# Kernel tuning notes

Measured on AMD Instinct MI355X. Metric: run time of the kernel, lower is better.

The kernel has to match this reference:

```python
import jax, jax.numpy as jnp
import numpy as np

B, C, H, W = 4, 96, 48, 48
N_STATE = 16
EXPAND = 2
D_INNER = EXPAND * C          # 192
DT_RANK = -(-C // 16)         # ceil(96/16) = 6
K = 4                         # 4 scan directions (VMamba cross-scan)
CA_R = 16                     # channel-attention reduction


def _ln(x, g, b, eps=1e-5):
    m = jnp.mean(x, -1, keepdims=True)
    v = jnp.mean((x - m) ** 2, -1, keepdims=True)
    return (x - m) * jax.lax.rsqrt(v + eps) * g + b


def setup_inputs() -> dict:
    key = jax.random.key(0)
    ks = jax.random.split(key, 12)
    f = lambda k, s, scale=0.02: jax.random.normal(k, s, dtype=jnp.float32) * scale
    # dt bias init per SS2D.dt_init: inv_dt = dt + log(-expm1(-dt))
    dt0 = jnp.exp(jax.random.uniform(ks[7], (K, D_INNER)) * (np.log(0.1) - np.log(1e-3)) + np.log(1e-3))
    dt_b = dt0 + jnp.log(-jnp.expm1(-dt0))
    A_logs = jnp.log(jnp.tile(jnp.arange(1, N_STATE + 1, dtype=jnp.float32)[None, :], (K * D_INNER, 1)))
    return {
        "x": jax.random.normal(ks[0], (B, C, H, W), dtype=jnp.float32),
        "ca_w1": f(ks[1], (C // CA_R, C), 0.1),
        "ca_w2": f(ks[2], (C, C // CA_R), 0.1),
        "ln_g": jnp.ones((C,), jnp.float32),
        "ln_b": jnp.zeros((C,), jnp.float32),
        "in_proj_w": f(ks[3], (2 * D_INNER, C)),
        "conv_w": f(ks[4], (D_INNER, 1, 3, 3), 0.1),
        "conv_b": jnp.zeros((D_INNER,), jnp.float32),
        "x_proj_w": f(ks[5], (K, DT_RANK + 2 * N_STATE, D_INNER)),
        "dt_w": f(ks[6], (K, D_INNER, DT_RANK), DT_RANK ** -0.5),
        "dt_b": dt_b,
        "A_logs": A_logs,
        "Ds": jnp.ones((K * D_INNER,), jnp.float32),
        "onorm_g": jnp.ones((D_INNER,), jnp.float32),
        "onorm_b": jnp.zeros((D_INNER,), jnp.float32),
        "out_proj_w": f(ks[8], (C, D_INNER)),
    }


def reference(x, ca_w1, ca_w2, ln_g, ln_b, in_proj_w, conv_w, conv_b,
              x_proj_w, dt_w, dt_b, A_logs, Ds, onorm_g, onorm_b, out_proj_w):
    # --- channel attention (SE-style) gating the encoder features ---
    s = x.mean((2, 3))                                    # [B,C]
    a = jax.nn.sigmoid(jax.nn.relu(s @ ca_w1.T) @ ca_w2.T)
    x_ca = x * a[:, :, None, None]

    # --- VSSBlock: LN -> SS2D -> residual ---
    xi = jnp.transpose(x_ca, (0, 2, 3, 1))               # [B,H,W,C]
    xn = _ln(xi, ln_g, ln_b)

    # SS2D in_proj, split x/z
    xz = xn @ in_proj_w.T                                 # [B,H,W,2*D]
    xc, z = jnp.split(xz, 2, axis=-1)

    # depthwise conv + SiLU
    xc = jnp.transpose(xc, (0, 3, 1, 2))                  # [B,D,H,W]
    xc = jax.lax.conv_general_dilated(
        xc, conv_w, (1, 1), 'SAME', feature_group_count=D_INNER,
        dimension_numbers=('NCHW', 'OIHW', 'NCHW')) + conv_b[None, :, None, None]
    xc = jax.nn.silu(xc)

    Bb, D, Hh, Ww = xc.shape
    L = Hh * Ww
    # cross-scan: hw, wh, and their reverses -> [B,4,D,L]
    x_hw = xc.reshape(Bb, D, L)
    x_wh = jnp.transpose(xc, (0, 1, 3, 2)).reshape(Bb, D, L)
    xs = jnp.stack([x_hw, x_wh], axis=1)
    xs = jnp.concatenate([xs, jnp.flip(xs, axis=-1)], axis=1)

    x_dbl = jnp.einsum('bkdl,kcd->bkcl', xs, x_proj_w)    # [B,4,R+2N,L]
    dts, Bs, Cs = jnp.split(x_dbl, [DT_RANK, DT_RANK + N_STATE], axis=2)
    dt = jnp.einsum('bkrl,kdr->bkdl', dts, dt_w)
    dt = jax.nn.softplus(dt + dt_b[None, :, :, None])     # [B,4,D,L]
    A = -jnp.exp(A_logs).reshape(K, D, N_STATE)           # [4,D,N]

    # selective scan over L (sequential recurrence, vectorized over B,K,D,N)
    dt_t = jnp.moveaxis(dt, -1, 0)                        # [L,B,4,D]
    B_t = jnp.moveaxis(Bs, -1, 0)                         # [L,B,4,N]
    C_t = jnp.moveaxis(Cs, -1, 0)
    u_t = jnp.moveaxis(xs, -1, 0)                         # [L,B,4,D]
    h0 = jnp.zeros((Bb, K, D, N_STATE), xc.dtype)

    def step(h, inp):
        dti, Bi, Ci, ui = inp
        h = h * jnp.exp(dti[..., None] * A) + (dti * ui)[..., None] * Bi[:, :, None, :]
        return h, jnp.einsum('bkdn,bkn->bkd', h, Ci)

    _, ys = jax.lax.scan(step, h0, (dt_t, B_t, C_t, u_t))
    ys = jnp.moveaxis(ys, 0, -1) + Ds.reshape(K, D)[None, :, :, None] * xs  # [B,4,D,L]

    # merge 4 directions back to hw order
    y_fwd, y_inv = ys[:, :2], jnp.flip(ys[:, 2:], axis=-1)

    def wh_to_hw(t):
        return jnp.transpose(t.reshape(Bb, D, Ww, Hh), (0, 1, 3, 2)).reshape(Bb, D, L)

    y = y_fwd[:, 0] + y_inv[:, 0] + wh_to_hw(y_fwd[:, 1]) + wh_to_hw(y_inv[:, 1])
    y = jnp.transpose(y.reshape(Bb, D, Hh, Ww), (0, 2, 3, 1))  # [B,H,W,D]
    y = _ln(y, onorm_g, onorm_b)
    y = y * jax.nn.silu(z)
    out = y @ out_proj_w.T                                # [B,H,W,C]
    out = xi + out                                        # VSSBlock residual
    return jnp.transpose(out, (0, 3, 1, 2))               # [B,C,H,W]
```

## Files before the change

### kernel.cpp

```cpp
#include <hip/hip_runtime.h>
#include <math.h>

#define Bn 4
#define Cc 96
#define Hh 48
#define Ww 48
#define HW 2304
#define Dd 192
#define NS 16
#define Kk 4
#define RK 6
#define CD 38
#define Ll 2304
#define NCH 64
#define CL 36
#define SU2S 72

typedef _Float16 half2v __attribute__((ext_vector_type(2)));
typedef _Float16 half4 __attribute__((ext_vector_type(4)));
typedef _Float16 half8 __attribute__((ext_vector_type(8)));
typedef float f4v __attribute__((ext_vector_type(4)));
typedef float f4raw __attribute__((ext_vector_type(4)));

#define FMA4(A,W,U) { A.x=fmaf(W,U.x,A.x); A.y=fmaf(W,U.y,A.y); A.z=fmaf(W,U.z,A.z); A.w=fmaf(W,U.w,A.w); }

__device__ __forceinline__ float sigmoidf_(float x){ return 1.0f/(1.0f+__expf(-x)); }
__device__ __forceinline__ float siluf_(float x){ return x*sigmoidf_(x); }
__device__ __forceinline__ float softplus_fast(float x){ return (x>15.0f)? x : __logf(1.0f+__expf(x)); }

__device__ __forceinline__ float dot2f(half2v a, half2v b, float c){
#if __has_builtin(__builtin_amdgcn_fdot2)
  return __builtin_amdgcn_fdot2(a, b, c, false);
#else
  return fmaf((float)a[1],(float)b[1], fmaf((float)a[0],(float)b[0], c));
#endif
}

__global__ __launch_bounds__(256) void k_mean(const float* __restrict__ x, float* __restrict__ s){
  int bc = blockIdx.x;
  const float* p = x + (size_t)bc*HW;
  float acc = 0.f;
  for(int i=threadIdx.x;i<HW;i+=256) acc += p[i];
  __shared__ float red[256];
  red[threadIdx.x]=acc; __syncthreads();
  for(int o=128;o>0;o>>=1){ if(threadIdx.x<o) red[threadIdx.x]+=red[threadIdx.x+o]; __syncthreads(); }
  if(threadIdx.x==0) s[bc]=red[0]*(1.0f/HW);
}

__global__ __launch_bounds__(384) void k_ca(const float* __restrict__ s, const float* __restrict__ w1,
                     const float* __restrict__ w2, float* __restrict__ a){
  __shared__ float hid[Bn*RK];
  int tid=threadIdx.x;
  if(tid<Bn*RK){
    int b=tid/RK, r=tid%RK;
    float acc=0.f;
    for(int c=0;c<Cc;c++) acc += s[b*Cc+c]*w1[r*Cc+c];
    hid[tid]=fmaxf(acc,0.f);
  }
  __syncthreads();
  int b=tid/Cc, c=tid%Cc;
  float acc=0.f;
  for(int r=0;r<RK;r++) acc += hid[b*RK+r]*w2[c*RK+r];
  a[tid]=sigmoidf_(acc);
}

__global__ __launch_bounds__(256) void k_xca(const float* __restrict__ x, const float* __restrict__ a,
                      float* __restrict__ xi){
  __shared__ float tile[32][65];
  int p0 = blockIdx.x*64, c0 = blockIdx.y*32, b = blockIdx.z;
  int pj = threadIdx.x%64, ci = threadIdx.x/64;
  for(int i=0;i<8;i++){
    int c = c0+ci+i*4;
    tile[ci+i*4][pj] = x[((size_t)(b*Cc+c))*HW + p0+pj]*a[b*Cc+c];
  }
  __syncthreads();
  int cl = threadIdx.x%32, pl = threadIdx.x/32;
  for(int i=0;i<8;i++){
    int p = pl + i*8;
    xi[((size_t)(b*HW + p0+p))*Cc + c0+cl] = tile[cl][p];
  }
}

__global__ __launch_bounds__(256) void k_lnproj(const float* __restrict__ xi,
    const float* __restrict__ g, const float* __restrict__ bta,
    const float* __restrict__ w, float* __restrict__ xc, float* __restrict__ z){
  __shared__ float su[Cc*36];
  __shared__ _Float16 wl16[128*104];
  int tid = threadIdx.x;
  int pix0 = blockIdx.x*32;
  int p = blockIdx.y;
  #pragma unroll
  for(int i=0;i<3;i++){
    int f4 = tid + 256*i;
    int px = f4/24, c4 = f4%24;
    float4 v = *(const float4*)(xi + (size_t)(pix0+px)*Cc + 4*c4);
    int sw = 4*(c4&7);
    su[(4*c4+0)*36 + (px^sw)] = v.x;
    su[(4*c4+1)*36 + (px^sw)] = v.y;
    su[(4*c4+2)*36 + (px^sw)] = v.z;
    su[(4*c4+3)*36 + (px^sw)] = v.w;
  }
  __syncthreads();
  {
    int px = tid>>3, gg = tid&7;
    float sm=0.f, sq=0.f;
    float vals[12];
    #pragma unroll
    for(int i=0;i<12;i++){
      int d = gg + 8*i;
      float v = su[d*36 + (px ^ (4*((d>>2)&7)))];
      vals[i]=v; sm+=v; sq+=v*v;
    }
    sm += __shfl_xor(sm,1); sq += __shfl_xor(sq,1);
    sm += __shfl_xor(sm,2); sq += __shfl_xor(sq,2);
    sm += __shfl_xor(sm,4); sq += __shfl_xor(sq,4);
    float mean = sm*(1.0f/Cc);
    float var  = sq*(1.0f/Cc) - mean*mean;
    float rs = rsqrtf(var + 1e-5f);
    #pragma unroll
    for(int i=0;i<12;i++){
      int d = gg + 8*i;
      su[d*36 + (px ^ (4*((d>>2)&7)))] = (vals[i]-mean)*rs*g[d] + bta[d];
    }
  }
  #pragma unroll
  for(int i=0;i<12;i++){
    int f4 = tid + 256*i;
    int r = f4/24, c4 = f4%24;
    float4 v = *(const float4*)(w + (size_t)(128*p + r)*Cc + 4*c4);
    half4 hv; hv[0]=(_Float16)v.x; hv[1]=(_Float16)v.y; hv[2]=(_Float16)v.z; hv[3]=(_Float16)v.w;
    *(half4*)(wl16 + r*104 + 4*c4) = hv;
  }
  __syncthreads();
  int t4 = tid&7, cg = tid>>3;
  float4 a0={0,0,0,0},a1={0,0,0,0},a2={0,0,0,0},a3={0,0,0,0};
  for(int d0=0; d0<Cc; d0+=8){
    half8 w0v = *(const half8*)(wl16 + (cg+  0)*104 + d0);
    half8 w1v = *(const half8*)(wl16 + (cg+ 32)*104 + d0);
    half8 w2v = *(const half8*)(wl16 + (cg+ 64)*104 + d0);
    half8 w3v = *(const half8*)(wl16 + (cg+ 96)*104 + d0);
    #pragma unroll
    for(int j=0;j<8;j++){
      int d = d0+j;
      float4 u4 = *(const float4*)(su + d*36 + 4*(t4 ^ ((d>>2)&7)));
      FMA4(a0,(float)w0v[j],u4);
      FMA4(a1,(float)w1v[j],u4);
      FMA4(a2,(float)w2v[j],u4);
      FMA4(a3,(float)w3v[j],u4);
    }
  }
  #pragma unroll
  for(int j=0;j<4;j++){
    int c = 128*p + cg + 32*j;
    float4 a = (j==0)?a0:(j==1)?a1:(j==2)?a2:a3;
    #pragma unroll
    for(int q=0;q<4;q++){
      int px = pix0 + 4*t4 + q;
      float vv = (q==0)?a.x:(q==1)?a.y:(q==2)?a.z:a.w;
      if(c < Dd) xc[(size_t)px*Dd + c] = vv;
      else       z [(size_t)px*Dd + (c-Dd)] = vv;
    }
  }
}

__global__ __launch_bounds__(256) void k_conv(const float* __restrict__ xc, const float* __restrict__ cw,
                       const float* __restrict__ cb, float* __restrict__ xo){
  int idx = blockIdx.x*256 + threadIdx.x;
  if(idx >= Bn*HW*(Dd/4)) return;
  int d4 = idx % (Dd/4); int pos = (idx/(Dd/4))%HW; int b = idx/((Dd/4)*HW);
  int h = pos/Ww, w = pos%Ww;
  int d0 = d4*4;
  float4 acc = {cb[d0],cb[d0+1],cb[d0+2],cb[d0+3]};
  #pragma unroll
  for(int kh=0;kh<3;kh++){
    int hh=h+kh-1; if(hh<0||hh>=Hh) continue;
    #pragma unroll
    for(int kw=0;kw<3;kw++){
      int ww2=w+kw-1; if(ww2<0||ww2>=Ww) continue;
      float4 v = *(const float4*)(xc + ((size_t)(b*HW + hh*Ww+ww2))*Dd + d0);
      int wi = kh*3+kw;
      acc.x += v.x*cw[(d0+0)*9+wi];
      acc.y += v.y*cw[(d0+1)*9+wi];
      acc.z += v.z*cw[(d0+2)*9+wi];
      acc.w += v.w*cw[(d0+3)*9+wi];
    }
  }
  float4 o; o.x=siluf_(acc.x); o.y=siluf_(acc.y); o.z=siluf_(acc.z); o.w=siluf_(acc.w);
  *(float4*)(xo + ((size_t)(b*HW+pos))*Dd + d0) = o;
}

__global__ __launch_bounds__(256) void k_xdbl(const float* __restrict__ xconv,
   const float* __restrict__ xpw, const float* __restrict__ dtw,
   const float* __restrict__ dtb, _Float16* __restrict__ dtC,
   _Float16* __restrict__ uC, _Float16* __restrict__ BC){
  __shared__ _Float16 su2[96*SU2S];
  __shared__ _Float16 wl16[CD*200];
  __shared__ float dts[RK*36];
  int tid = threadIdx.x;
  int blk = blockIdx.x;
  int tile = blk % (Ll/32);
  int k    = (blk/(Ll/32))%Kk;
  int b    = blk/((Ll/32)*Kk);
  int ord  = k&1;
  bool rev = (k>=2);
  int t0 = tile*32;
  #pragma unroll
  for(int i=0;i<6;i++){
    int f4 = tid+256*i;
    int r = f4/48, c4 = f4%48;
    int t = t0+r;
    int pos = ord ? ((t%Ww)*Ww + t/Ww) : t;
    float4 v = *(const float4*)(xconv + (size_t)(b*HW+pos)*Dd + 4*c4);
    int dp0 = 2*c4;
    int off = ((r>>2) ^ (c4&7))*8 + (r&3)*2;
    half2v p0; p0[0]=(_Float16)v.x; p0[1]=(_Float16)v.y;
    half2v p1; p1[0]=(_Float16)v.z; p1[1]=(_Float16)v.w;
    *(half2v*)(su2 + dp0*SU2S + off) = p0;
    *(half2v*)(su2 + (dp0+1)*SU2S + off) = p1;
    if(k<2){
      half4 hv; hv[0]=(_Float16)v.x; hv[1]=(_Float16)v.y; hv[2]=(_Float16)v.z; hv[3]=(_Float16)v.w;
      *(half4*)(uC + ((size_t)(b*2+ord)*Ll + t)*Dd + 4*c4) = hv;
    }
  }
  for(int i=tid;i<CD*48;i+=256){
    int c = i/48, c4 = i%48;
    float4 v = *(const float4*)(xpw + ((size_t)(k*CD+c))*Dd + 4*c4);
    half4 hv; hv[0]=(_Float16)v.x; hv[1]=(_Float16)v.y; hv[2]=(_Float16)v.z; hv[3]=(_Float16)v.w;
    *(half4*)(wl16 + c*200 + 4*c4) = hv;
  }
  __syncthreads();
  int t4 = tid&7, cg = tid>>3;
  bool has1 = (cg < CD-32);
  f4v a0={0,0,0,0}, a1={0,0,0,0};
  #pragma unroll 1
  for(int dpc=0; dpc<24; dpc++){
    f4raw w0r = *(const f4raw*)(wl16 + cg*200 + 8*dpc);
    f4raw w1r = {0.f,0.f,0.f,0.f};
    if(has1) w1r = *(const f4raw*)(wl16 + (cg+32)*200 + 8*dpc);
    #pragma unroll
    for(int j=0;j<4;j++){
      int dp = 4*dpc+j;
      f4raw ur = *(const f4raw*)(su2 + dp*SU2S + (t4 ^ ((dp>>1)&7))*8);
      half2v w0p = __builtin_bit_cast(half2v, w0r[j]);
      half2v w1p = __builtin_bit_cast(half2v, w1r[j]);
      #pragma unroll
      for(int q=0;q<4;q++){
        half2v up = __builtin_bit_cast(half2v, ur[q]);
        a0[q] = dot2f(up, w0p, a0[q]);
        if(has1) a1[q] = dot2f(up, w1p, a1[q]);
      }
    }
  }
  #pragma unroll
  for(int j=0;j<2;j++){
    if(j==1 && !has1) break;
    int c = cg + 32*j;
    f4v a = j? a1 : a0;
    if(c < RK){
      dts[c*36 + 4*t4+0]=a[0]; dts[c*36+4*t4+1]=a[1]; dts[c*36+4*t4+2]=a[2]; dts[c*36+4*t4+3]=a[3];
    } else {
      int nn = c - RK;
      _Float16* dst = BC + ((size_t)(b*Kk+k)*Ll)*32 + nn;
      #pragma unroll
      for(int q=0;q<4;q++){
        int t = t0 + 4*t4 + q;
        int tq = rev ? (Ll-1-t) : t;
        dst[(size_t)tq*32] = (_Float16)a[q];
      }
    }
  }
  __syncthreads();
  {
    int tl = tid&31, ds8 = tid>>5;
    #pragma unroll 4
    for(int i=0;i<24;i++){
      int d = ds8 + 8*i;
      float acc = dtb[k*Dd + d];
      #pragma unroll
      for(int r=0;r<RK;r++) acc = fmaf(dtw[((size_t)(k*Dd+d))*RK + r], dts[r*36 + tl], acc);
      wl16[tl*200 + d] = (_Float16)softplus_fast(acc);
    }
  }
  __syncthreads();
  {
    _Float16* dbase = dtC + (size_t)(b*Kk+k)*Ll*Dd;
    #pragma unroll
    for(int i=0;i<3;i++){
      int f8 = tid + 256*i;
      int row = f8/24, c8 = f8%24;
      int t = t0+row;
      int tq = rev ? (Ll-1-t) : t;
      *(half8*)(dbase + (size_t)tq*Dd + 8*c8) = *(const half8*)(wl16 + row*200 + 8*c8);
    }
  }
}

__global__ __launch_bounds__(192) void k_scan1(const _Float16* __restrict__ dtC,
  const _Float16* __restrict__ uC, const _Float16* __restrict__ BC,
  const float* __restrict__ Alog, _Float16* __restrict__ hloc, _Float16* __restrict__ Pb){
  int blk=blockIdx.x;
  int ch  = blk%NCH;
  int k   = (blk/NCH)%Kk;
  int b   = blk/(NCH*Kk);
  int d = threadIdx.x;
  const float* ap = Alog + ((size_t)(k*Dd+d))*NS;
  float An[16];
  #pragma unroll
  for(int i=0;i<16;i++) An[i] = -__expf(ap[i]);
  const _Float16* dp = dtC + (size_t)(b*Kk+k)*Ll*Dd + d;
  const _Float16* up = uC  + (size_t)(b*2+(k&1))*Ll*Dd + d;
  const _Float16* bc = BC  + ((size_t)(b*Kk+k)*Ll + ch*CL)*32;
  bool rev = (k>=2);
  int s0 = ch*CL;
  float h[16];
  #pragma unroll
  for(int i=0;i<16;i++) h[i]=0.f;
  float sdt = 0.f;
  #pragma unroll 1
  for(int tl=0; tl<CL; tl+=4){
    float dtv4[4], uv[4];
    #pragma unroll
    for(int j=0;j<4;j++){
      dtv4[j] = (float)dp[(size_t)(s0+tl+j)*Dd];
      int ut = rev ? (Ll-1-s0-tl-j) : (s0+tl+j);
      uv[j]  = (float)up[(size_t)ut*Dd];
    }
    #pragma unroll
    for(int j=0;j<4;j++){
      half8 B0 = *(const half8*)(bc + (size_t)(tl+j)*32);
      half8 B1 = *(const half8*)(bc + (size_t)(tl+j)*32 + 8);
      float dtv = dtv4[j];
      sdt += dtv;
      float xB = dtv*uv[j];
      #pragma unroll
      for(int i=0;i<8;i++){
        float ae = __expf(dtv*An[i]);
        h[i] = fmaf(h[i], ae, xB*(float)B0[i]);
      }
      #pragma unroll
      for(int i=0;i<8;i++){
        float ae = __expf(dtv*An[8+i]);
        h[8+i] = fmaf(h[8+i], ae, xB*(float)B1[i]);
      }
    }
  }
  size_t o = (((size_t)(b*Kk+k)*NCH + ch)*Dd + d)*NS;
  half8 ho0, ho1;
  #pragma unroll
  for(int i=0;i<8;i++){ ho0[i]=(_Float16)h[i]; ho1[i]=(_Float16)h[8+i]; }
  *(half8*)(hloc+o) = ho0; *(half8*)(hloc+o+8) = ho1;
  half8 po0, po1;
  #pragma unroll
  for(int i=0;i<8;i++){ po0[i]=(_Float16)__expf(An[i]*sdt); po1[i]=(_Float16)__expf(An[8+i]*sdt); }
  *(half8*)(Pb+o) = po0; *(half8*)(Pb+o+8) = po1;
}

__global__ __launch_bounds__(256) void k_comb(_Float16* __restrict__ hloc,
  const _Float16* __restrict__ Pb){
  int idx = blockIdx.x*256 + threadIdx.x;
  int inner = idx % (Dd*NS);
  int bk = idx / (Dd*NS);
  size_t base = (size_t)bk*NCH*Dd*NS + inner;
  float H = 0.f;
  for(int ch=0; ch<NCH; ch++){
    size_t o = base + (size_t)ch*Dd*NS;
    float hl = (float)hloc[o];
    hloc[o] = (_Float16)H;
    H = (float)Pb[o]*H + hl;
  }
}

__global__ __launch_bounds__(192) void k_scan2(const _Float16* __restrict__ dtC,
  const _Float16* __restrict__ uC, const _Float16* __restrict__ BC,
  const float* __restrict__ Alog, const float* __restrict__ Ds,
  const _Float16* __restrict__ Hin, _Float16* __restrict__ yB){
  int blk=blockIdx.x;
  int ch  = blk%NCH;
  int k   = (blk/NCH)%Kk;
  int b   = blk/(NCH*Kk);
  int d = threadIdx.x;
  const float* ap = Alog + ((size_t)(k*Dd+d))*NS;
  float An[16];
  #pragma unroll
  for(int i=0;i<16;i++) An[i] = -__expf(ap[i]);
  float Dv = Ds[k*Dd+d];
  const _Float16* dp = dtC + (size_t)(b*Kk+k)*Ll*Dd + d;
  const _Float16* up = uC  + (size_t)(b*2+(k&1))*Ll*Dd + d;
  const _Float16* bc = BC  + ((size_t)(b*Kk+k)*Ll + ch*CL)*32;
  bool rev = (k>=2);
  int s0 = ch*CL;
  const _Float16* hp = Hin + (((size_t)(b*Kk+k)*NCH + ch)*Dd + d)*NS;
  float h[16];
  {
    half8 h0=*(const half8*)(hp), h1=*(const half8*)(hp+8);
    #pragma unroll
    for(int i=0;i<8;i++){ h[i]=(float)h0[i]; h[8+i]=(float)h1[i]; }
  }
  _Float16* yp = yB + ((size_t)(b*Kk+k)*Ll + s0)*Dd + d;
  #pragma unroll 1
  for(int tl=0; tl<CL; tl+=4){
    float dtv4[4], uv[4];
    #pragma unroll
    for(int j=0;j<4;j++){
      dtv4[j] = (float)dp[(size_t)(s0+tl+j)*Dd];
      int ut = rev ? (Ll-1-s0-tl-j) : (s0+tl+j);
      uv[j]  = (float)up[(size_t)ut*Dd];
    }
    #pragma unroll
    for(int j=0;j<4;j++){
      half8 B0 = *(const half8*)(bc + (size_t)(tl+j)*32);
      half8 B1 = *(const half8*)(bc + (size_t)(tl+j)*32 + 8);
      half8 C0 = *(const half8*)(bc + (size_t)(tl+j)*32 + 16);
      half8 C1 = *(const half8*)(bc + (size_t)(tl+j)*32 + 24);
      float dtv = dtv4[j];
      float xB = dtv*uv[j];
      float p = 0.f;
      #pragma unroll
      for(int i=0;i<8;i++){
        float ae = __expf(dtv*An[i]);
        h[i] = fmaf(h[i], ae, xB*(float)B0[i]);
        p = fmaf(h[i], (float)C0[i], p);
      }
      #pragma unroll
      for(int i=0;i<8;i++){
        float ae = __expf(dtv*An[8+i]);
        h[8+i] = fmaf(h[8+i], ae, xB*(float)B1[i]);
        p = fmaf(h[8+i], (float)C1[i], p);
      }
      yp[(size_t)(tl+j)*Dd] = (_Float16)(p + Dv*uv[j]);
    }
  }
}

__global__ __launch_bounds__(256) void k_merge(const _Float16* __restrict__ yB,
  const float* __restrict__ og, const float* __restrict__ ob,
  const float* __restrict__ zB, const float* __restrict__ opw,
  const float* __restrict__ xi, float* __restrict__ ot){
  __shared__ float yv[Dd*36];
  __shared__ _Float16 wl16[48*200];
  int tid = threadIdx.x;
  int pix0 = blockIdx.x*32;
  int p = blockIdx.y;
  int b = pix0/HW;
  int pos0 = pix0%HW;
  size_t ybase = (size_t)b*Kk*Ll*Dd;
  #pragma unroll
  for(int i=0;i<3;i++){
    int f8 = tid+256*i;
    int r = f8/24, c8 = f8%24;
    int pos = pos0+r;
    int lwh = (pos%Ww)*Ww + pos/Ww;
    half8 v0 = *(const half8*)(yB + ybase + ((size_t)(0*Ll) + pos)*Dd + 8*c8);
    half8 v2 = *(const half8*)(yB + ybase + ((size_t)(2*Ll) + (Ll-1-pos))*Dd + 8*c8);
    half8 v1 = *(const half8*)(yB + ybase + ((size_t)(1*Ll) + lwh)*Dd + 8*c8);
    half8 v3 = *(const half8*)(yB + ybase + ((size_t)(3*Ll) + (Ll-1-lwh))*Dd + 8*c8);
    #pragma unroll
    for(int j=0;j<8;j++){
      int d = 8*c8+j;
      float vs = (float)v0[j]+(float)v1[j]+(float)v2[j]+(float)v3[j];
      yv[d*36 + (r ^ (4*((d>>2)&7)))] = vs;
    }
  }
  for(int i=tid;i<48*48;i+=256){
    int c=i/48, c4=i%48;
    float4 v = *(const float4*)(opw + (size_t)(48*p+c)*Dd + 4*c4);
    half4 hv; hv[0]=(_Float16)v.x; hv[1]=(_Float16)v.y; hv[2]=(_Float16)v.z; hv[3]=(_Float16)v.w;
    *(half4*)(wl16 + c*200 + 4*c4) = hv;
  }
  __syncthreads();
  {
    int px = tid>>3, gg = tid&7;
    float sm=0.f, sq=0.f;
    float vals[24];
    #pragma unroll
    for(int i=0;i<24;i++){
      int d = gg + 8*i;
      float v = yv[d*36 + (px ^ (4*((d>>2)&7)))];
      vals[i]=v; sm+=v; sq+=v*v;
    }
    sm += __shfl_xor(sm,1); sq += __shfl_xor(sq,1);
    sm += __shfl_xor(sm,2); sq += __shfl_xor(sq,2);
    sm += __shfl_xor(sm,4); sq += __shfl_xor(sq,4);
    float mean = sm*(1.0f/Dd);
    float var  = sq*(1.0f/Dd) - mean*mean;
    float rs = rsqrtf(var + 1e-5f);
    #pragma unroll
    for(int i=0;i<24;i++){
      int d = gg + 8*i;
      float zv = zB[(size_t)(pix0+px)*Dd + d];
      yv[d*36 + (px ^ (4*((d>>2)&7)))] = ((vals[i]-mean)*rs*og[d] + ob[d]) * siluf_(zv);
    }
  }
  __syncthreads();
  int t4 = tid&7, cg = tid>>3;
  bool h1 = (cg < 16);
  float4 a0={0,0,0,0}, a1={0,0,0,0};
  for(int d0=0;d0<Dd;d0+=8){
    half8 w0v = *(const half8*)(wl16 + cg*200 + d0);
    half8 w1v;
    if(h1) w1v = *(const half8*)(wl16 + (cg+32)*200 + d0);
    #pragma unroll
    for(int j=0;j<8;j++){
      int d=d0+j;
      float4 u4 = *(const float4*)(yv + d*36 + 4*(t4 ^ ((d>>2)&7)));
      FMA4(a0,(float)w0v[j],u4);
      if(h1){ FMA4(a1,(float)w1v[j],u4); }
    }
  }
  #pragma unroll
  for(int j=0;j<2;j++){
    if(j==1 && !h1) break;
    int c = 48*p + cg + 32*j;
    float4 a = j?a1:a0;
    #pragma unroll
    for(int q=0;q<4;q++){
      int px = pix0 + 4*t4 + q;
      float vv = (q==0)?a.x:(q==1)?a.y:(q==2)?a.z:a.w;
      ot[(size_t)px*Cc + c] = vv + xi[(size_t)px*Cc + c];
    }
  }
}

__global__ __launch_bounds__(256) void k_outT(const float* __restrict__ ot, float* __restrict__ out){
  __shared__ float tile[64][33];
  int p0=blockIdx.x*64, c0=blockIdx.y*32, b=blockIdx.z;
  int cl=threadIdx.x%32, pl=threadIdx.x/32;
  for(int i=0;i<8;i++){
    int p = pl+i*8;
    tile[p][cl] = ot[((size_t)(b*HW+p0+p))*Cc + c0+cl];
  }
  __syncthreads();
  int pj=threadIdx.x%64, ci=threadIdx.x/64;
  for(int i=0;i<8;i++){
    int c=ci+i*4;
    out[((size_t)(b*Cc+c0+c))*HW + p0+pj] = tile[pj][c];
  }
}

extern "C" void kernel_launch(void* const* d_in, const int* in_sizes, int n_in,
                              void* d_out, int out_size, void* d_ws, size_t ws_size,
                              hipStream_t stream){
  const float* x   = (const float*)d_in[0];
  const float* cw1 = (const float*)d_in[1];
  const float* cw2 = (const float*)d_in[2];
  const float* lng = (const float*)d_in[3];
  const float* lnb = (const float*)d_in[4];
  const float* ipw = (const float*)d_in[5];
  const float* cvw = (const float*)d_in[6];
  const float* cvb = (const float*)d_in[7];
  const float* xpw = (const float*)d_in[8];
  const float* dtw = (const float*)d_in[9];
  const float* dtb = (const float*)d_in[10];
  const float* alg = (const float*)d_in[11];
  const float* ds  = (const float*)d_in[12];
  const float* ong = (const float*)d_in[13];
  const float* onb = (const float*)d_in[14];
  const float* opw = (const float*)d_in[15];
  float* out = (float*)d_out;
  float* ws = (float*)d_ws;

  float* s_   = ws;
  float* a_   = s_  + 384;
  float* xi_  = a_  + 384;
  float* xc_  = xi_ + 884736;
  float* z_   = xc_ + 1769472;
  float* xo_  = z_  + 1769472;
  _Float16* dtC_ = (_Float16*)(xo_ + 1769472);
  _Float16* uC_  = dtC_ + 7077888;
  _Float16* BC_  = uC_ + 3538944;
  _Float16* yB_  = BC_ + 1179648;
  float* ot_  = (float*)(yB_ + 7077888);

  _Float16* hloc_ = (_Float16*)xc_;
  _Float16* Pb_   = (_Float16*)xo_;

  k_mean  <<<Bn*Cc, 256, 0, stream>>>(x, s_);
  k_ca    <<<1, 384, 0, stream>>>(s_, cw1, cw2, a_);
  k_xca   <<<dim3(HW/64, Cc/32, Bn), 256, 0, stream>>>(x, a_, xi_);
  k_lnproj<<<dim3(Bn*HW/32, 3), 256, 0, stream>>>(xi_, lng, lnb, ipw, xc_, z_);
  k_conv  <<<(Bn*HW*(Dd/4))/256, 256, 0, stream>>>(xc_, cvw, cvb, xo_);
  k_xdbl  <<<Bn*Kk*(Ll/32), 256, 0, stream>>>(xo_, xpw, dtw, dtb, dtC_, uC_, BC_);
  k_scan1 <<<Bn*Kk*NCH, 192, 0, stream>>>(dtC_, uC_, BC_, alg, hloc_, Pb_);
  k_comb  <<<(Bn*Kk*Dd*NS)/256, 256, 0, stream>>>(hloc_, Pb_);
  k_scan2 <<<Bn*Kk*NCH, 192, 0, stream>>>(dtC_, uC_, BC_, alg, ds, hloc_, yB_);
  k_merge <<<dim3(Bn*HW/32, 2), 256, 0, stream>>>(yB_, ong, onb, z_, opw, xi_, ot_);
  k_outT  <<<dim3(HW/64, Cc/32, Bn), 256, 0, stream>>>(ot_, out);
}
```

Baseline: 181.1 us.

## Store intermediates in fp16, drop uC copy, fuse output transpose into merge

```diff
diff --git a/kernel.cpp b/kernel.cpp
--- a/kernel.cpp
+++ b/kernel.cpp
@@ -83,7 +83,7 @@
 
 __global__ __launch_bounds__(256) void k_lnproj(const float* __restrict__ xi,
     const float* __restrict__ g, const float* __restrict__ bta,
-    const float* __restrict__ w, float* __restrict__ xc, float* __restrict__ z){
+    const float* __restrict__ w, _Float16* __restrict__ xc, _Float16* __restrict__ z){
   __shared__ float su[Cc*36];
   __shared__ _Float16 wl16[128*104];
   int tid = threadIdx.x;
@@ -157,42 +157,44 @@
     for(int q=0;q<4;q++){
       int px = pix0 + 4*t4 + q;
       float vv = (q==0)?a.x:(q==1)?a.y:(q==2)?a.z:a.w;
-      if(c < Dd) xc[(size_t)px*Dd + c] = vv;
-      else       z [(size_t)px*Dd + (c-Dd)] = vv;
-    }
-  }
-}
-
-__global__ __launch_bounds__(256) void k_conv(const float* __restrict__ xc, const float* __restrict__ cw,
-                       const float* __restrict__ cb, float* __restrict__ xo){
+      if(c < Dd) xc[(size_t)px*Dd + c] = (_Float16)vv;
+      else       z [(size_t)px*Dd + (c-Dd)] = (_Float16)vv;
+    }
+  }
+}
+
+__global__ __launch_bounds__(256) void k_conv(const _Float16* __restrict__ xc, const float* __restrict__ cw,
+                       const float* __restrict__ cb, _Float16* __restrict__ xo){
   int idx = blockIdx.x*256 + threadIdx.x;
-  if(idx >= Bn*HW*(Dd/4)) return;
-  int d4 = idx % (Dd/4); int pos = (idx/(Dd/4))%HW; int b = idx/((Dd/4)*HW);
+  if(idx >= Bn*HW*(Dd/8)) return;
+  int d8 = idx % (Dd/8); int pos = (idx/(Dd/8))%HW; int b = idx/((Dd/8)*HW);
   int h = pos/Ww, w = pos%Ww;
-  int d0 = d4*4;
-  float4 acc = {cb[d0],cb[d0+1],cb[d0+2],cb[d0+3]};
+  int d0 = d8*8;
+  float acc[8];
+  #pragma unroll
+  for(int j=0;j<8;j++) acc[j]=cb[d0+j];
   #pragma unroll
   for(int kh=0;kh<3;kh++){
     int hh=h+kh-1; if(hh<0||hh>=Hh) continue;
     #pragma unroll
     for(int kw=0;kw<3;kw++){
       int ww2=w+kw-1; if(ww2<0||ww2>=Ww) continue;
-      float4 v = *(const float4*)(xc + ((size_t)(b*HW + hh*Ww+ww2))*Dd + d0);
+      half8 v = *(const half8*)(xc + ((size_t)(b*HW + hh*Ww+ww2))*Dd + d0);
       int wi = kh*3+kw;
-      acc.x += v.x*cw[(d0+0)*9+wi];
-      acc.y += v.y*cw[(d0+1)*9+wi];
-      acc.z += v.z*cw[(d0+2)*9+wi];
-      acc.w += v.w*cw[(d0+3)*9+wi];
-    }
-  }
-  float4 o; o.x=siluf_(acc.x); o.y=siluf_(acc.y); o.z=siluf_(acc.z); o.w=siluf_(acc.w);
-  *(float4*)(xo + ((size_t)(b*HW+pos))*Dd + d0) = o;
-}
-
-__global__ __launch_bounds__(256) void k_xdbl(const float* __restrict__ xconv,
+      #pragma unroll
+      for(int j=0;j<8;j++) acc[j] = fmaf((float)v[j], cw[(d0+j)*9+wi], acc[j]);
+    }
+  }
+  half8 o;
+  #pragma unroll
+  for(int j=0;j<8;j++) o[j] = (_Float16)siluf_(acc[j]);
+  *(half8*)(xo + ((size_t)(b*HW+pos))*Dd + d0) = o;
+}
+
+__global__ __launch_bounds__(256) void k_xdbl(const _Float16* __restrict__ xoH,
    const float* __restrict__ xpw, const float* __restrict__ dtw,
    const float* __restrict__ dtb, _Float16* __restrict__ dtC,
-   _Float16* __restrict__ uC, _Float16* __restrict__ BC){
+   _Float16* __restrict__ BC){
   __shared__ _Float16 su2[96*SU2S];
   __shared__ _Float16 wl16[CD*200];
   __shared__ float dts[RK*36];
@@ -205,22 +207,22 @@
   bool rev = (k>=2);
   int t0 = tile*32;
   #pragma unroll
-  for(int i=0;i<6;i++){
-    int f4 = tid+256*i;
-    int r = f4/48, c4 = f4%48;
+  for(int i=0;i<3;i++){
+    int f8 = tid+256*i;
+    int r = f8/24, c8 = f8%24;
     int t = t0+r;
     int pos = ord ? ((t%Ww)*Ww + t/Ww) : t;
-    float4 v = *(const float4*)(xconv + (size_t)(b*HW+pos)*Dd + 4*c4);
-    int dp0 = 2*c4;
-    int off = ((r>>2) ^ (c4&7))*8 + (r&3)*2;
-    half2v p0; p0[0]=(_Float16)v.x; p0[1]=(_Float16)v.y;
-    half2v p1; p1[0]=(_Float16)v.z; p1[1]=(_Float16)v.w;
-    *(half2v*)(su2 + dp0*SU2S + off) = p0;
-    *(half2v*)(su2 + (dp0+1)*SU2S + off) = p1;
-    if(k<2){
-      half4 hv; hv[0]=(_Float16)v.x; hv[1]=(_Float16)v.y; hv[2]=(_Float16)v.z; hv[3]=(_Float16)v.w;
-      *(half4*)(uC + ((size_t)(b*2+ord)*Ll + t)*Dd + 4*c4) = hv;
-    }
+    half8 hv = *(const half8*)(xoH + (size_t)(b*HW+pos)*Dd + 8*c8);
+    int c4a = 2*c8, c4b = 2*c8+1;
+    int offa = ((r>>2) ^ (c4a&7))*8 + (r&3)*2;
+    int offb = ((r>>2) ^ (c4b&7))*8 + (r&3)*2;
+    half2v p0,p1,p2,p3;
+    p0[0]=hv[0];p0[1]=hv[1]; p1[0]=hv[2];p1[1]=hv[3];
+    p2[0]=hv[4];p2[1]=hv[5]; p3[0]=hv[6];p3[1]=hv[7];
+    *(half2v*)(su2 + (4*c8+0)*SU2S + offa) = p0;
+    *(half2v*)(su2 + (4*c8+1)*SU2S + offa) = p1;
+    *(half2v*)(su2 + (4*c8+2)*SU2S + offb) = p2;
+    *(half2v*)(su2 + (4*c8+3)*SU2S + offb) = p3;
   }
   for(int i=tid;i<CD*48;i+=256){
     int c = i/48, c4 = i%48;
@@ -296,19 +298,20 @@
 }
 
 __global__ __launch_bounds__(192) void k_scan1(const _Float16* __restrict__ dtC,
-  const _Float16* __restrict__ uC, const _Float16* __restrict__ BC,
+  const _Float16* __restrict__ xoH, const _Float16* __restrict__ BC,
   const float* __restrict__ Alog, _Float16* __restrict__ hloc, _Float16* __restrict__ Pb){
   int blk=blockIdx.x;
   int ch  = blk%NCH;
   int k   = (blk/NCH)%Kk;
   int b   = blk/(NCH*Kk);
   int d = threadIdx.x;
+  int ord = k&1;
   const float* ap = Alog + ((size_t)(k*Dd+d))*NS;
   float An[16];
   #pragma unroll
   for(int i=0;i<16;i++) An[i] = -__expf(ap[i]);
   const _Float16* dp = dtC + (size_t)(b*Kk+k)*Ll*Dd + d;
-  const _Float16* up = uC  + (size_t)(b*2+(k&1))*Ll*Dd + d;
+  const _Float16* up = xoH + (size_t)b*HW*Dd + d;
   const _Float16* bc = BC  + ((size_t)(b*Kk+k)*Ll + ch*CL)*32;
   bool rev = (k>=2);
   int s0 = ch*CL;
@@ -323,7 +326,8 @@
     for(int j=0;j<4;j++){
       dtv4[j] = (float)dp[(size_t)(s0+tl+j)*Dd];
       int ut = rev ? (Ll-1-s0-tl-j) : (s0+tl+j);
-      uv[j]  = (float)up[(size_t)ut*Dd];
+      int pos = ord ? ((ut%Ww)*Ww + ut/Ww) : ut;
+      uv[j]  = (float)up[(size_t)pos*Dd];
     }
     #pragma unroll
     for(int j=0;j<4;j++){
@@ -371,7 +375,7 @@
 }
 
 __global__ __launch_bounds__(192) void k_scan2(const _Float16* __restrict__ dtC,
-  const _Float16* __restrict__ uC, const _Float16* __restrict__ BC,
+  const _Float16* __restrict__ xoH, const _Float16* __restrict__ BC,
   const float* __restrict__ Alog, const float* __restrict__ Ds,
   const _Float16* __restrict__ Hin, _Float16* __restrict__ yB){
   int blk=blockIdx.x;
@@ -379,13 +383,14 @@
   int k   = (blk/NCH)%Kk;
   int b   = blk/(NCH*Kk);
   int d = threadIdx.x;
+  int ord = k&1;
   const float* ap = Alog + ((size_t)(k*Dd+d))*NS;
   float An[16];
   #pragma unroll
   for(int i=0;i<16;i++) An[i] = -__expf(ap[i]);
   float Dv = Ds[k*Dd+d];
   const _Float16* dp = dtC + (size_t)(b*Kk+k)*Ll*Dd + d;
-  const _Float16* up = uC  + (size_t)(b*2+(k&1))*Ll*Dd + d;
+  const _Float16* up = xoH + (size_t)b*HW*Dd + d;
   const _Float16* bc = BC  + ((size_t)(b*Kk+k)*Ll + ch*CL)*32;
   bool rev = (k>=2);
   int s0 = ch*CL;
@@ -404,7 +409,8 @@
     for(int j=0;j<4;j++){
       dtv4[j] = (float)dp[(size_t)(s0+tl+j)*Dd];
       int ut = rev ? (Ll-1-s0-tl-j) : (s0+tl+j);
-      uv[j]  = (float)up[(size_t)ut*Dd];
+      int pos = ord ? ((ut%Ww)*Ww + ut/Ww) : ut;
+      uv[j]  = (float)up[(size_t)pos*Dd];
     }
     #pragma unroll
     for(int j=0;j<4;j++){
@@ -434,8 +440,8 @@
 
 __global__ __launch_bounds__(256) void k_merge(const _Float16* __restrict__ yB,
   const float* __restrict__ og, const float* __restrict__ ob,
-  const float* __restrict__ zB, const float* __restrict__ opw,
-  const float* __restrict__ xi, float* __restrict__ ot){
+  const _Float16* __restrict__ zB, const float* __restrict__ opw,
+  const float* __restrict__ xi, float* __restrict__ out){
   __shared__ float yv[Dd*36];
   __shared__ _Float16 wl16[48*200];
   int tid = threadIdx.x;
@@ -487,7 +493,7 @@
     #pragma unroll
     for(int i=0;i<24;i++){
       int d = gg + 8*i;
-      float zv = zB[(size_t)(pix0+px)*Dd + d];
+      float zv = (float)zB[(size_t)(pix0+px)*Dd + d];
       yv[d*36 + (px ^ (4*((d>>2)&7)))] = ((vals[i]-mean)*rs*og[d] + ob[d]) * siluf_(zv);
     }
   }
@@ -512,28 +518,12 @@
     if(j==1 && !h1) break;
     int c = 48*p + cg + 32*j;
     float4 a = j?a1:a0;
-    #pragma unroll
-    for(int q=0;q<4;q++){
-      int px = pix0 + 4*t4 + q;
-      float vv = (q==0)?a.x:(q==1)?a.y:(q==2)?a.z:a.w;
-      ot[(size_t)px*Cc + c] = vv + xi[(size_t)px*Cc + c];
-    }
-  }
-}
-
-__global__ __launch_bounds__(256) void k_outT(const float* __restrict__ ot, float* __restrict__ out){
-  __shared__ float tile[64][33];
-  int p0=blockIdx.x*64, c0=blockIdx.y*32, b=blockIdx.z;
-  int cl=threadIdx.x%32, pl=threadIdx.x/32;
-  for(int i=0;i<8;i++){
-    int p = pl+i*8;
-    tile[p][cl] = ot[((size_t)(b*HW+p0+p))*Cc + c0+cl];
-  }
-  __syncthreads();
-  int pj=threadIdx.x%64, ci=threadIdx.x/64;
-  for(int i=0;i<8;i++){
-    int c=ci+i*4;
-    out[((size_t)(b*Cc+c0+c))*HW + p0+pj] = tile[pj][c];
+    float4 r;
+    r.x = a.x + xi[(size_t)(pix0 + 4*t4 + 0)*Cc + c];
+    r.y = a.y + xi[(size_t)(pix0 + 4*t4 + 1)*Cc + c];
+    r.z = a.z + xi[(size_t)(pix0 + 4*t4 + 2)*Cc + c];
+    r.w = a.w + xi[(size_t)(pix0 + 4*t4 + 3)*Cc + c];
+    *(float4*)(out + (size_t)(b*Cc + c)*HW + pos0 + 4*t4) = r;
   }
 }
 
@@ -562,27 +552,23 @@
   float* s_   = ws;
   float* a_   = s_  + 384;
   float* xi_  = a_  + 384;
-  float* xc_  = xi_ + 884736;
-  float* z_   = xc_ + 1769472;
-  float* xo_  = z_  + 1769472;
-  _Float16* dtC_ = (_Float16*)(xo_ + 1769472);
-  _Float16* uC_  = dtC_ + 7077888;
-  _Float16* BC_  = uC_ + 3538944;
-  _Float16* yB_  = BC_ + 1179648;
-  float* ot_  = (float*)(yB_ + 7077888);
-
-  _Float16* hloc_ = (_Float16*)xc_;
-  _Float16* Pb_   = (_Float16*)xo_;
+  _Float16* xcH_ = (_Float16*)(xi_ + 884736);
+  _Float16* zH_  = xcH_ + 1769472;
+  _Float16* xoH_ = zH_  + 1769472;
+  _Float16* dtC_ = xoH_ + 1769472;
+  _Float16* BC_  = dtC_ + 7077888;
+  _Float16* yB_  = BC_  + 1179648;
+  _Float16* hloc_= yB_  + 7077888;
+  _Float16* Pb_  = hloc_+ 3145728;
 
   k_mean  <<<Bn*Cc, 256, 0, stream>>>(x, s_);
   k_ca    <<<1, 384, 0, stream>>>(s_, cw1, cw2, a_);
   k_xca   <<<dim3(HW/64, Cc/32, Bn), 256, 0, stream>>>(x, a_, xi_);
-  k_lnproj<<<dim3(Bn*HW/32, 3), 256, 0, stream>>>(xi_, lng, lnb, ipw, xc_, z_);
-  k_conv  <<<(Bn*HW*(Dd/4))/256, 256, 0, stream>>>(xc_, cvw, cvb, xo_);
-  k_xdbl  <<<Bn*Kk*(Ll/32), 256, 0, stream>>>(xo_, xpw, dtw, dtb, dtC_, uC_, BC_);
-  k_scan1 <<<Bn*Kk*NCH, 192, 0, stream>>>(dtC_, uC_, BC_, alg, hloc_, Pb_);
+  k_lnproj<<<dim3(Bn*HW/32, 3), 256, 0, stream>>>(xi_, lng, lnb, ipw, xcH_, zH_);
+  k_conv  <<<(Bn*HW*(Dd/8))/256, 256, 0, stream>>>(xcH_, cvw, cvb, xoH_);
+  k_xdbl  <<<Bn*Kk*(Ll/32), 256, 0, stream>>>(xoH_, xpw, dtw, dtb, dtC_, BC_);
+  k_scan1 <<<Bn*Kk*NCH, 192, 0, stream>>>(dtC_, xoH_, BC_, alg, hloc_, Pb_);
   k_comb  <<<(Bn*Kk*Dd*NS)/256, 256, 0, stream>>>(hloc_, Pb_);
-  k_scan2 <<<Bn*Kk*NCH, 192, 0, stream>>>(dtC_, uC_, BC_, alg, ds, hloc_, yB_);
-  k_merge <<<dim3(Bn*HW/32, 2), 256, 0, stream>>>(yB_, ong, onb, z_, opw, xi_, ot_);
-  k_outT  <<<dim3(HW/64, Cc/32, Bn), 256, 0, stream>>>(ot_, out);
-}
+  k_scan2 <<<Bn*Kk*NCH, 192, 0, stream>>>(dtC_, xoH_, BC_, alg, ds, hloc_, yB_);
+  k_merge <<<dim3(Bn*HW/32, 2), 256, 0, stream>>>(yB_, ong, onb, zH_, opw, xi_, out);
+}
```

After: 190.1 us. 1.05x slower.
